# Kernel optimization log

Hardware: AMD Instinct MI355X
Metric: run time of the kernel (lower is better)

## Reference

```python
import jax, jax.numpy as jnp
import numpy as np

N = 100000
E = 1600000
D_IN = 128
D_H = 128


def _sage_conv(x, src, dst, W_self, W_neigh, b, n_nodes):
    # mean aggregation over in-neighbors: dst receives from src
    gathered = x[src]                                        # [E, D]
    summed = jax.ops.segment_sum(gathered, dst, num_segments=n_nodes)  # [N, D]
    deg = jax.ops.segment_sum(jnp.ones((src.shape[0],), x.dtype), dst,
                              num_segments=n_nodes)          # [N]
    mean_neigh = summed / jnp.maximum(deg, 1.0)[:, None]     # zero-degree -> 0
    return x @ W_self + mean_neigh @ W_neigh + b


def setup_inputs() -> dict:
    key = jax.random.key(0)
    ks = jax.random.split(key, 9)
    s1 = 1.0 / np.sqrt(D_IN)
    s2 = 1.0 / np.sqrt(D_H)
    return {
        "in_feat": jax.random.normal(ks[0], (N, D_IN), jnp.float32),
        "W1_self": jax.random.uniform(ks[1], (D_IN, D_H), jnp.float32, -s1, s1),
        "W1_neigh": jax.random.uniform(ks[2], (D_IN, D_H), jnp.float32, -s1, s1),
        "b1": jnp.zeros((D_H,), jnp.float32),
        "W2_self": jax.random.uniform(ks[3], (D_H, D_H), jnp.float32, -s2, s2),
        "W2_neigh": jax.random.uniform(ks[4], (D_H, D_H), jnp.float32, -s2, s2),
        "b2": jnp.zeros((D_H,), jnp.float32),
        "src": jax.random.randint(ks[5], (E,), 0, N, jnp.int32),
        "dst": jax.random.randint(ks[6], (E,), 0, N, jnp.int32),
    }


def reference(in_feat, W1_self, W1_neigh, b1, W2_self, W2_neigh, b2, src, dst):
    h = _sage_conv(in_feat, src, dst, W1_self, W1_neigh, b1, N)
    h = jax.nn.relu(h)
    h = _sage_conv(h, src, dst, W2_self, W2_neigh, b2, N)
    return h
```

## Files before the change

### kernel.cpp

```cpp
#include <hip/hip_runtime.h>
#include <hip/hip_fp16.h>

#define D 128
#define NB_MAX 1024
#define PART_BLOCKS 512

using f32x4  = __attribute__((ext_vector_type(4))) float;
using half8  = __attribute__((ext_vector_type(8))) _Float16;
using short8 = __attribute__((ext_vector_type(8))) short;

#define AS1(p) ((const __attribute__((address_space(1))) void*)(p))
#define AS3(p) ((__attribute__((address_space(3))) void*)(p))

__global__ void prep_k(const float* __restrict__ x, __half* __restrict__ y, int n4,
                       const float* __restrict__ W1s, const float* __restrict__ W1n,
                       const float* __restrict__ W2s, const float* __restrict__ W2n,
                       unsigned short* __restrict__ Wg1, unsigned short* __restrict__ Wg2,
                       int* __restrict__ bucket_counts, int nb, int xb) {
    int b = blockIdx.x;
    int t = threadIdx.x;
    if (b < xb) {
        int i = b * 256 + t;
        if (i < n4) {
            float4 v = *(const float4*)(x + (size_t)i * 4);
            __half2 h0 = __floats2half2_rn(v.x, v.y);
            __half2 h1 = __floats2half2_rn(v.z, v.w);
            __half2* o = (__half2*)(y + (size_t)i * 4);
            o[0] = h0; o[1] = h1;
        }
        return;
    }
    int wb = b - xb;
    if (wb < 512) {
        int sel = wb >> 8;
        int lb  = wb & 255;
        if (lb >= 128) return;
        const float* Ws = sel ? W2s : W1s;
        const float* Wn = sel ? W2n : W1n;
        unsigned short* Wg = sel ? Wg2 : Wg1;
        int idx = lb * 256 + t;
        int col = idx >> 8;
        int k   = idx & 255;
        float v = (k < 128) ? Ws[k * D + col] : Wn[(k - 128) * D + col];
        _Float16 hv = (_Float16)v;
        _Float16 lv = (_Float16)(v - (float)hv);
        int kc = k >> 5, q = (k >> 3) & 3, j = k & 7;
        Wg[(((kc * 2 + 0) * 4 + q) * 128 + col) * 8 + j] = *(unsigned short*)&hv;
        Wg[(((kc * 2 + 1) * 4 + q) * 128 + col) * 8 + j] = *(unsigned short*)&lv;
        return;
    }
    int i = (wb - 512) * 256 + t;
    if (i < nb) bucket_counts[i] = 0;
}

__global__ void bucket_count_k(const int* __restrict__ dst, int* __restrict__ bucket_counts,
                               int E, int nb) {
    __shared__ int hist[NB_MAX];
    int t = threadIdx.x;
    for (int b = t; b < nb; b += 256) hist[b] = 0;
    __syncthreads();
    for (int i = blockIdx.x * 256 + t; i < E; i += gridDim.x * 256)
        atomicAdd(&hist[dst[i] >> 8], 1);
    __syncthreads();
    for (int b = t; b < nb; b += 256) {
        int c = hist[b];
        if (c) atomicAdd(&bucket_counts[b], c);
    }
}

__global__ void bucket_scan_k(const int* __restrict__ bucket_counts,
                              int* __restrict__ bucket_base,
                              int* __restrict__ bucket_cursor, int nb) {
    __shared__ int sh[256];
    int t = threadIdx.x;
    int base = t * 4;
    int v0 = (base + 0 < nb) ? bucket_counts[base + 0] : 0;
    int v1 = (base + 1 < nb) ? bucket_counts[base + 1] : 0;
    int v2 = (base + 2 < nb) ? bucket_counts[base + 2] : 0;
    int v3 = (base + 3 < nb) ? bucket_counts[base + 3] : 0;
    int tsum = v0 + v1 + v2 + v3;
    sh[t] = tsum;
    __syncthreads();
    for (int off = 1; off < 256; off <<= 1) {
        int x = 0;
        if (t >= off) x = sh[t - off];
        __syncthreads();
        if (t >= off) sh[t] += x;
        __syncthreads();
    }
    int excl = sh[t] - tsum;
    if (base + 0 < nb) { bucket_base[base+0] = excl;          bucket_cursor[base+0] = excl; }
    if (base + 1 < nb) { bucket_base[base+1] = excl+v0;       bucket_cursor[base+1] = excl+v0; }
    if (base + 2 < nb) { bucket_base[base+2] = excl+v0+v1;    bucket_cursor[base+2] = excl+v0+v1; }
    if (base + 3 < nb) { bucket_base[base+3] = excl+v0+v1+v2; bucket_cursor[base+3] = excl+v0+v1+v2; }
    if (t == 255) bucket_base[nb] = sh[255];
}

__global__ void partition_k(const int* __restrict__ src, const int* __restrict__ dst,
                            int* __restrict__ bucket_cursor, unsigned* __restrict__ pairs,
                            int E, int nb, int chunk) {
    __shared__ int hist[NB_MAX];
    __shared__ int bbase[NB_MAX];
    int t = threadIdx.x;
    int e0 = blockIdx.x * chunk;
    int e1 = min(E, e0 + chunk);
    for (int b = t; b < nb; b += 256) hist[b] = 0;
    __syncthreads();
    for (int i = e0 + t; i < e1; i += 256)
        atomicAdd(&hist[dst[i] >> 8], 1);
    __syncthreads();
    for (int b = t; b < nb; b += 256) {
        int c = hist[b];
        int bs = 0;
        if (c) bs = atomicAdd(&bucket_cursor[b], c);
        bbase[b] = bs;
        hist[b] = 0;
    }
    __syncthreads();
    for (int i = e0 + t; i < e1; i += 256) {
        int dd = dst[i];
        int b = dd >> 8;
        int r = atomicAdd(&hist[b], 1);
        pairs[bbase[b] + r] = ((unsigned)(dd & 255) << 17) | (unsigned)src[i];
    }
}

__global__ void build_csr_k(const unsigned* __restrict__ pairs,
                            const int* __restrict__ bucket_base,
                            int* __restrict__ counts, int* __restrict__ offsets,
                            int* __restrict__ edge_src, int N) {
    __shared__ int hist[256];
    __shared__ int curs[256];
    __shared__ int sh[256];
    int t = threadIdx.x;
    int b = blockIdx.x;
    int n0 = b << 8;
    int e0 = bucket_base[b];
    int e1 = bucket_base[b + 1];
    hist[t] = 0;
    __syncthreads();
    for (int i = e0 + t; i < e1; i += 256)
        atomicAdd(&hist[pairs[i] >> 17], 1);
    __syncthreads();
    int c = hist[t];
    sh[t] = c;
    __syncthreads();
    for (int off = 1; off < 256; off <<= 1) {
        int x = 0;
        if (t >= off) x = sh[t - off];
        __syncthreads();
        if (t >= off) sh[t] += x;
        __syncthreads();
    }
    int excl = sh[t] - c;
    curs[t] = excl;
    int node = n0 + t;
    if (node < N) { counts[node] = c; offsets[node] = e0 + excl; }
    __syncthreads();
    for (int i = e0 + t; i < e1; i += 256) {
        unsigned p = pairs[i];
        int pos = atomicAdd(&curs[p >> 17], 1);
        edge_src[e0 + pos] = (int)(p & 0x1FFFFu);
    }
}

__global__ void aggregate_f16_k(const __half* __restrict__ x,
                                const int* __restrict__ edge_src,
                                const int* __restrict__ offsets,
                                const int* __restrict__ counts,
                                __half* __restrict__ agg, int n) {
    int wid  = (blockIdx.x * blockDim.x + threadIdx.x) >> 6;
    int lane = threadIdx.x & 63;
    if (wid >= n) return;
    int sg  = lane >> 4;
    int sub = lane & 15;
    int start = offsets[wid];
    int cnt   = counts[wid];
    float acc[8] = {0.f, 0.f, 0.f, 0.f, 0.f, 0.f, 0.f, 0.f};
    for (int base = 0; base < cnt; base += 64) {
        int valid = min(64, cnt - base);
        int s = (lane < valid) ? edge_src[start + base + lane] : 0;
        for (int k0 = 0; k0 < valid; k0 += 16) {
            float4 raw[4];
            float  wg[4];
            #pragma unroll
            for (int u = 0; u < 4; ++u) {
                int idx = k0 + 4 * u + sg;
                int row = __shfl(s, idx & 63);
                wg[u] = (idx < valid) ? 1.0f : 0.0f;
                raw[u] = *(const float4*)(x + (size_t)row * D + sub * 8);
            }
            #pragma unroll
            for (int u = 0; u < 4; ++u) {
                const __half2* hp = (const __half2*)&raw[u];
                #pragma unroll
                for (int j = 0; j < 4; ++j) {
                    float2 f = __half22float2(hp[j]);
                    acc[2 * j]     = fmaf(f.x, wg[u], acc[2 * j]);
                    acc[2 * j + 1] = fmaf(f.y, wg[u], acc[2 * j + 1]);
                }
            }
        }
    }
    #pragma unroll
    for (int j = 0; j < 8; ++j) {
        acc[j] += __shfl(acc[j], lane ^ 16);
        acc[j] += __shfl(acc[j], lane ^ 32);
    }
    if (sg == 0) {
        float inv = 1.0f / fmaxf((float)cnt, 1.0f);
        union { __half2 h2[4]; short8 s8; } u;
        #pragma unroll
        for (int j = 0; j < 4; ++j)
            u.h2[j] = __floats2half2_rn(acc[2 * j] * inv, acc[2 * j + 1] * inv);
        *(short8*)(agg + (size_t)wid * D + sub * 8) = u.s8;
    }
}

__global__ __launch_bounds__(512)
void mfma_gemm_k(const _Float16* __restrict__ A0, const _Float16* __restrict__ A1,
                 const unsigned short* __restrict__ Wg,
                 const float* __restrict__ bias,
                 float* __restrict__ C, __half* __restrict__ Ch,
                 int n, int out_mode) {
    __shared__ __align__(16) unsigned short lds_b[8192];
    int t = threadIdx.x;
    int w = t >> 6;
    int l = t & 63;
    int m = l & 15;
    int q = l >> 4;
    int r0 = blockIdx.x * 256 + w * 32;

    f32x4 acc[2][8];
    #pragma unroll
    for (int rt = 0; rt < 2; ++rt)
        #pragma unroll
        for (int ct = 0; ct < 8; ++ct)
            acc[rt][ct] = (f32x4){0.f, 0.f, 0.f, 0.f};

    for (int kc = 0; kc < 8; ++kc) {
        const unsigned short* gk = Wg + (size_t)kc * 8192;
        #pragma unroll
        for (int i = 0; i < 2; ++i) {
            int e = i * 512 + t;
            __builtin_amdgcn_global_load_lds(AS1(gk + e * 8), AS3(lds_b + e * 8), 16, 0, 0);
        }
        const _Float16* __restrict__ A = (kc < 4) ? A0 : A1;
        int ka = (kc & 3) * 32;
        half8 a[2];
        #pragma unroll
        for (int rt = 0; rt < 2; ++rt) {
            int row = r0 + rt * 16 + m;
            half8 v = (half8){0, 0, 0, 0, 0, 0, 0, 0};
            if (row < n) v = *(const half8*)(A + (size_t)row * D + ka + q * 8);
            a[rt] = v;
        }
        __syncthreads();

        #pragma unroll
        for (int ct = 0; ct < 8; ++ct) {
            half8 bh = *(const half8*)&lds_b[(size_t)(q * 128 + ct * 16 + m) * 8];
            half8 bl = *(const half8*)&lds_b[(size_t)((4 + q) * 128 + ct * 16 + m) * 8];
            #pragma unroll
            for (int rt = 0; rt < 2; ++rt) {
                acc[rt][ct] = __builtin_amdgcn_mfma_f32_16x16x32_f16(a[rt], bh, acc[rt][ct], 0, 0, 0);
                acc[rt][ct] = __builtin_amdgcn_mfma_f32_16x16x32_f16(a[rt], bl, acc[rt][ct], 0, 0, 0);
            }
        }
        __syncthreads();
    }

    #pragma unroll
    for (int ct = 0; ct < 8; ++ct) {
        int col = ct * 16 + m;
        float bb = bias[col];
        #pragma unroll
        for (int rt = 0; rt < 2; ++rt) {
            #pragma unroll
            for (int r = 0; r < 4; ++r) {
                int row = r0 + rt * 16 + q * 4 + r;
                if (row < n) {
                    float v = acc[rt][ct][r] + bb;
                    if (out_mode) {
                        v = fmaxf(v, 0.f);
                        Ch[(size_t)row * D + col] = __float2half(v);
                    } else {
                        C[(size_t)row * D + col] = v;
                    }
                }
            }
        }
    }
}

extern "C" void kernel_launch(void* const* d_in, const int* in_sizes, int n_in,
                              void* d_out, int out_size, void* d_ws, size_t ws_size,
                              hipStream_t stream) {
    const float* in_feat = (const float*)d_in[0];
    const float* W1s     = (const float*)d_in[1];
    const float* W1n     = (const float*)d_in[2];
    const float* b1      = (const float*)d_in[3];
    const float* W2s     = (const float*)d_in[4];
    const float* W2n     = (const float*)d_in[5];
    const float* b2      = (const float*)d_in[6];
    const int*   src     = (const int*)d_in[7];
    const int*   dst     = (const int*)d_in[8];

    const int N  = in_sizes[0] / D;
    const int E  = in_sizes[7];
    const int NB = (N + 255) >> 8;

    char* base = (char*)d_ws;
    size_t off = 0;
    __half* agg16 = (__half*)(base + off); off += (size_t)N * D * 2;
    __half* xh16  = (__half*)(base + off); off += (size_t)N * D * 2;
    int* edge_src = (int*)(base + off);    off += (size_t)E * 4;
    int* counts   = (int*)(base + off);    off += (size_t)N * 4;
    int* offsets  = (int*)(base + off);    off += (size_t)N * 4;
    unsigned short* Wg1 = (unsigned short*)(base + off); off += 65536 * 2;
    unsigned short* Wg2 = (unsigned short*)(base + off); off += 65536 * 2;
    int* bucket_counts = (int*)(base + off); off += NB_MAX * 4;
    int* bucket_base   = (int*)(base + off); off += (NB_MAX + 1) * 4;
    off = (off + 15) & ~(size_t)15;
    int* bucket_cursor = (int*)(base + off); off += NB_MAX * 4;

    unsigned* pairs = (unsigned*)agg16;

    const int chunk = (E + PART_BLOCKS - 1) / PART_BLOCKS;
    const int n4 = (N * D) / 4;
    const int xb = (n4 + 255) / 256;
    const int zb = (NB + 255) / 256;

    hipLaunchKernelGGL(prep_k, dim3(xb + 512 + zb), dim3(256), 0, stream,
                       in_feat, xh16, n4, W1s, W1n, W2s, W2n, Wg1, Wg2,
                       bucket_counts, NB, xb);

    hipLaunchKernelGGL(bucket_count_k, dim3(PART_BLOCKS), dim3(256), 0, stream,
                       dst, bucket_counts, E, NB);
    hipLaunchKernelGGL(bucket_scan_k, dim3(1), dim3(256), 0, stream,
                       bucket_counts, bucket_base, bucket_cursor, NB);
    hipLaunchKernelGGL(partition_k, dim3(PART_BLOCKS), dim3(256), 0, stream,
                       src, dst, bucket_cursor, pairs, E, NB, chunk);
    hipLaunchKernelGGL(build_csr_k, dim3(NB), dim3(256), 0, stream,
                       pairs, bucket_base, counts, offsets, edge_src, N);

    const dim3 aggGrid(((size_t)N * 64 + 255) / 256);
    const dim3 gemmGrid((N + 255) / 256);

    hipLaunchKernelGGL(aggregate_f16_k, aggGrid, dim3(256), 0, stream,
                       xh16, edge_src, offsets, counts, agg16, N);
    hipLaunchKernelGGL(mfma_gemm_k, gemmGrid, dim3(512), 0, stream,
                       (const _Float16*)xh16, (const _Float16*)agg16, Wg1, b1,
                       (float*)nullptr, xh16, N, 1);

    hipLaunchKernelGGL(aggregate_f16_k, aggGrid, dim3(256), 0, stream,
                       xh16, edge_src, offsets, counts, agg16, N);
    hipLaunchKernelGGL(mfma_gemm_k, gemmGrid, dim3(512), 0, stream,
                       (const _Float16*)xh16, (const _Float16*)agg16, Wg2, b2,
                       (float*)d_out, (__half*)nullptr, N, 0);
}
```

Before: 352.0 us.

## Fuse bucket counting into prep kernel, pad zero row, use fma_mix in aggregation

```diff
diff --git a/kernel.cpp b/kernel.cpp
--- a/kernel.cpp
+++ b/kernel.cpp
@@ -4,6 +4,7 @@
 #define D 128
 #define NB_MAX 1024
 #define PART_BLOCKS 512
+#define CNT_BLOCKS 512
 
 using f32x4  = __attribute__((ext_vector_type(4))) float;
 using half8  = __attribute__((ext_vector_type(8))) _Float16;
@@ -11,30 +12,40 @@
 
 #define AS1(p) ((const __attribute__((address_space(1))) void*)(p))
 #define AS3(p) ((__attribute__((address_space(3))) void*)(p))
+
+#define FMA_MIX_LO(acc, dw, one) \
+    asm("v_fma_mix_f32 %0, %1, %2, %0 op_sel:[0,0,0] op_sel_hi:[1,0,0]" \
+        : "+v"(acc) : "v"(dw), "v"(one))
+#define FMA_MIX_HI(acc, dw, one) \
+    asm("v_fma_mix_f32 %0, %1, %2, %0 op_sel:[1,0,0] op_sel_hi:[1,0,0]" \
+        : "+v"(acc) : "v"(dw), "v"(one))
 
 __global__ void prep_k(const float* __restrict__ x, __half* __restrict__ y, int n4,
                        const float* __restrict__ W1s, const float* __restrict__ W1n,
                        const float* __restrict__ W2s, const float* __restrict__ W2n,
                        unsigned short* __restrict__ Wg1, unsigned short* __restrict__ Wg2,
-                       int* __restrict__ bucket_counts, int nb, int xb) {
+                       const int* __restrict__ dst, int* __restrict__ bucket_counts,
+                       int E, int nb, float* __restrict__ xpad) {
+    __shared__ int hist[NB_MAX];
     int b = blockIdx.x;
     int t = threadIdx.x;
-    if (b < xb) {
-        int i = b * 256 + t;
-        if (i < n4) {
-            float4 v = *(const float4*)(x + (size_t)i * 4);
-            __half2 h0 = __floats2half2_rn(v.x, v.y);
-            __half2 h1 = __floats2half2_rn(v.z, v.w);
-            __half2* o = (__half2*)(y + (size_t)i * 4);
-            o[0] = h0; o[1] = h1;
+    if (b < CNT_BLOCKS) {
+        if (b == 0 && t < 64) xpad[t] = 0.f;
+        for (int i = t; i < nb; i += 256) hist[i] = 0;
+        __syncthreads();
+        for (int i = b * 256 + t; i < E; i += CNT_BLOCKS * 256)
+            atomicAdd(&hist[dst[i] >> 8], 1);
+        __syncthreads();
+        for (int i = t; i < nb; i += 256) {
+            int c = hist[i];
+            if (c) atomicAdd(&bucket_counts[i], c);
         }
         return;
     }
-    int wb = b - xb;
-    if (wb < 512) {
-        int sel = wb >> 8;
-        int lb  = wb & 255;
-        if (lb >= 128) return;
+    int wb = b - CNT_BLOCKS;
+    if (wb < 256) {
+        int sel = wb >> 7;
+        int lb  = wb & 127;
         const float* Ws = sel ? W2s : W1s;
         const float* Wn = sel ? W2n : W1n;
         unsigned short* Wg = sel ? Wg2 : Wg1;
@@ -49,22 +60,13 @@
         Wg[(((kc * 2 + 1) * 4 + q) * 128 + col) * 8 + j] = *(unsigned short*)&lv;
         return;
     }
-    int i = (wb - 512) * 256 + t;
-    if (i < nb) bucket_counts[i] = 0;
-}
-
-__global__ void bucket_count_k(const int* __restrict__ dst, int* __restrict__ bucket_counts,
-                               int E, int nb) {
-    __shared__ int hist[NB_MAX];
-    int t = threadIdx.x;
-    for (int b = t; b < nb; b += 256) hist[b] = 0;
-    __syncthreads();
-    for (int i = blockIdx.x * 256 + t; i < E; i += gridDim.x * 256)
-        atomicAdd(&hist[dst[i] >> 8], 1);
-    __syncthreads();
-    for (int b = t; b < nb; b += 256) {
-        int c = hist[b];
-        if (c) atomicAdd(&bucket_counts[b], c);
+    int i = (b - CNT_BLOCKS - 256) * 256 + t;
+    if (i < n4) {
+        float4 v = *(const float4*)(x + (size_t)i * 4);
+        __half2 h0 = __floats2half2_rn(v.x, v.y);
+        __half2 h1 = __floats2half2_rn(v.z, v.w);
+        __half2* o = (__half2*)(y + (size_t)i * 4);
+        o[0] = h0; o[1] = h1;
     }
 }
 
@@ -127,7 +129,7 @@
 
 __global__ void build_csr_k(const unsigned* __restrict__ pairs,
                             const int* __restrict__ bucket_base,
-                            int* __restrict__ counts, int* __restrict__ offsets,
+                            int2* __restrict__ offcnt,
                             int* __restrict__ edge_src, int N) {
     __shared__ int hist[256];
     __shared__ int curs[256];
@@ -155,7 +157,7 @@
     int excl = sh[t] - c;
     curs[t] = excl;
     int node = n0 + t;
-    if (node < N) { counts[node] = c; offsets[node] = e0 + excl; }
+    if (node < N) offcnt[node] = make_int2(e0 + excl, c);
     __syncthreads();
     for (int i = e0 + t; i < e1; i += 256) {
         unsigned p = pairs[i];
@@ -166,38 +168,35 @@
 
 __global__ void aggregate_f16_k(const __half* __restrict__ x,
                                 const int* __restrict__ edge_src,
-                                const int* __restrict__ offsets,
-                                const int* __restrict__ counts,
+                                const int2* __restrict__ offcnt,
                                 __half* __restrict__ agg, int n) {
     int wid  = (blockIdx.x * blockDim.x + threadIdx.x) >> 6;
     int lane = threadIdx.x & 63;
     if (wid >= n) return;
     int sg  = lane >> 4;
     int sub = lane & 15;
-    int start = offsets[wid];
-    int cnt   = counts[wid];
+    int2 oc = offcnt[wid];
+    int start = oc.x;
+    int cnt   = oc.y;
+    float one = 1.0f;
     float acc[8] = {0.f, 0.f, 0.f, 0.f, 0.f, 0.f, 0.f, 0.f};
     for (int base = 0; base < cnt; base += 64) {
         int valid = min(64, cnt - base);
-        int s = (lane < valid) ? edge_src[start + base + lane] : 0;
+        int s = (lane < valid) ? edge_src[start + base + lane] : n;
         for (int k0 = 0; k0 < valid; k0 += 16) {
             float4 raw[4];
-            float  wg[4];
             #pragma unroll
             for (int u = 0; u < 4; ++u) {
-                int idx = k0 + 4 * u + sg;
-                int row = __shfl(s, idx & 63);
-                wg[u] = (idx < valid) ? 1.0f : 0.0f;
+                int row = __shfl(s, (k0 + 4 * u + sg) & 63);
                 raw[u] = *(const float4*)(x + (size_t)row * D + sub * 8);
             }
             #pragma unroll
             for (int u = 0; u < 4; ++u) {
-                const __half2* hp = (const __half2*)&raw[u];
+                const unsigned* dw = (const unsigned*)&raw[u];
                 #pragma unroll
                 for (int j = 0; j < 4; ++j) {
-                    float2 f = __half22float2(hp[j]);
-                    acc[2 * j]     = fmaf(f.x, wg[u], acc[2 * j]);
-                    acc[2 * j + 1] = fmaf(f.y, wg[u], acc[2 * j + 1]);
+                    FMA_MIX_LO(acc[2 * j],     dw[j], one);
+                    FMA_MIX_HI(acc[2 * j + 1], dw[j], one);
                 }
             }
         }
@@ -313,10 +312,9 @@
     char* base = (char*)d_ws;
     size_t off = 0;
     __half* agg16 = (__half*)(base + off); off += (size_t)N * D * 2;
-    __half* xh16  = (__half*)(base + off); off += (size_t)N * D * 2;
+    __half* xh16  = (__half*)(base + off); off += ((size_t)N * D + D) * 2;
     int* edge_src = (int*)(base + off);    off += (size_t)E * 4;
-    int* counts   = (int*)(base + off);    off += (size_t)N * 4;
-    int* offsets  = (int*)(base + off);    off += (size_t)N * 4;
+    int2* offcnt  = (int2*)(base + off);   off += (size_t)N * 8;
     unsigned short* Wg1 = (unsigned short*)(base + off); off += 65536 * 2;
     unsigned short* Wg2 = (unsigned short*)(base + off); off += 65536 * 2;
     int* bucket_counts = (int*)(base + off); off += NB_MAX * 4;
@@ -325,36 +323,36 @@
     int* bucket_cursor = (int*)(base + off); off += NB_MAX * 4;
 
     unsigned* pairs = (unsigned*)agg16;
+    float* xpad = (float*)(xh16 + (size_t)N * D);
 
     const int chunk = (E + PART_BLOCKS - 1) / PART_BLOCKS;
     const int n4 = (N * D) / 4;
     const int xb = (n4 + 255) / 256;
-    const int zb = (NB + 255) / 256;
-
-    hipLaunchKernelGGL(prep_k, dim3(xb + 512 + zb), dim3(256), 0, stream,
+
+    hipMemsetAsync(bucket_counts, 0, NB_MAX * 4, stream);
+
+    hipLaunchKernelGGL(prep_k, dim3(CNT_BLOCKS + 256 + xb), dim3(256), 0, stream,
                        in_feat, xh16, n4, W1s, W1n, W2s, W2n, Wg1, Wg2,
-                       bucket_counts, NB, xb);
-
-    hipLaunchKernelGGL(bucket_count_k, dim3(PART_BLOCKS), dim3(256), 0, stream,
-                       dst, bucket_counts, E, NB);
+                       dst, bucket_counts, E, NB, xpad);
+
     hipLaunchKernelGGL(bucket_scan_k, dim3(1), dim3(256), 0, stream,
                        bucket_counts, bucket_base, bucket_cursor, NB);
     hipLaunchKernelGGL(partition_k, dim3(PART_BLOCKS), dim3(256), 0, stream,
                        src, dst, bucket_cursor, pairs, E, NB, chunk);
     hipLaunchKernelGGL(build_csr_k, dim3(NB), dim3(256), 0, stream,
-                       pairs, bucket_base, counts, offsets, edge_src, N);
+                       pairs, bucket_base, offcnt, edge_src, N);
 
     const dim3 aggGrid(((size_t)N * 64 + 255) / 256);
     const dim3 gemmGrid((N + 255) / 256);
 
     hipLaunchKernelGGL(aggregate_f16_k, aggGrid, dim3(256), 0, stream,
-                       xh16, edge_src, offsets, counts, agg16, N);
+                       xh16, edge_src, offcnt, agg16, N);
     hipLaunchKernelGGL(mfma_gemm_k, gemmGrid, dim3(512), 0, stream,
                        (const _Float16*)xh16, (const _Float16*)agg16, Wg1, b1,
                        (float*)nullptr, xh16, N, 1);
 
     hipLaunchKernelGGL(aggregate_f16_k, aggGrid, dim3(256), 0, stream,
-                       xh16, edge_src, offsets, counts, agg16, N);
+                       xh16, edge_src, offcnt, agg16, N);
     hipLaunchKernelGGL(mfma_gemm_k, gemmGrid, dim3(512), 0, stream,
                        (const _Float16*)xh16, (const _Float16*)agg16, Wg2, b2,
                        (float*)d_out, (__half*)nullptr, N, 0);
```

After: 344.7 us. 1.02x faster.
